# Kernel optimization log

Hardware: AMD Instinct MI355X
Metric: run time of the kernel (lower is better)

## Reference

```python
import jax, jax.numpy as jnp
import numpy as np

B, T, D, H = 32, 4096, 512, 8
HD = D // H
SCALE = HD ** -0.5


def setup_inputs() -> dict:
    key = jax.random.key(0)
    ks = jax.random.split(key, 5)
    s = 0.02
    return {
        "enc": jax.random.normal(ks[0], (B, T, D), dtype=jnp.float32),
        "Wq": jax.random.normal(ks[1], (D, D), dtype=jnp.float32) * s,
        "Wk": jax.random.normal(ks[2], (D, D), dtype=jnp.float32) * s,
        "Wv": jax.random.normal(ks[3], (D, D), dtype=jnp.float32) * s,
        "Wo": jax.random.normal(ks[4], (D, D), dtype=jnp.float32) * s,
    }


def reference(enc, Wq, Wk, Wv, Wo):
    b, t, d = enc.shape
    # projections (torch Linear: y = x @ W.T)
    q = enc[:, -1, :] @ Wq.T                     # [B, D]
    k = (enc @ Wk.T).reshape(b, t, H, HD)        # [B, T, H, HD]
    v = (enc @ Wv.T).reshape(b, t, H, HD)        # [B, T, H, HD]
    q = q.reshape(b, H, HD)                      # [B, H, HD]
    scores = jnp.einsum('bhd,bthd->bht', q, k) * SCALE   # [B, H, T]
    weights = jax.nn.softmax(scores, axis=-1)             # [B, H, T]
    context = jnp.einsum('bht,bthd->bhd', weights, v)     # [B, H, HD]
    context = context.reshape(b, d) @ Wo.T                # [B, D]
    return (context, weights.mean(axis=1))
```

## Files before the change

### kernel.cpp

```cpp
#include <hip/hip_runtime.h>

#define BB 32
#define TT 4096
#define DD 512
#define HH 8
#define HDD 64
#define SCALE_F 0.125f
#define NCHS 64
#define CHUNKS 32
#define TC 128

__global__ __launch_bounds__(256) void k_qu(const float* __restrict__ enc,
                                            const float* __restrict__ Wq,
                                            const float* __restrict__ Wk,
                                            float* __restrict__ u) {
    __shared__ float x[DD];
    __shared__ float qh[HDD];
    int b = blockIdx.x >> 3, h = blockIdx.x & 7;
    int tid = threadIdx.x;
    const float* el = enc + ((size_t)b * TT + (TT - 1)) * DD;
    for (int i = tid; i < DD; i += 256) x[i] = el[i];
    __syncthreads();
    if (tid < HDD) {
        const float4* wr = (const float4*)(Wq + (size_t)(h * HDD + tid) * DD);
        float acc = 0.f;
#pragma unroll 4
        for (int d = 0; d < DD / 4; ++d) {
            float4 w = wr[d];
            acc += w.x * x[4 * d] + w.y * x[4 * d + 1] + w.z * x[4 * d + 2] + w.w * x[4 * d + 3];
        }
        qh[tid] = acc;
    }
    __syncthreads();
#pragma unroll
    for (int k = 0; k < 2; ++k) {
        int d = tid + 256 * k;
        float acc = 0.f;
#pragma unroll 8
        for (int j = 0; j < HDD; ++j)
            acc += qh[j] * Wk[(size_t)(h * HDD + j) * DD + d];
        u[(size_t)(b * HH + h) * DD + d] = acc * SCALE_F;
    }
}

__global__ __launch_bounds__(256) void k_sexp(const float* __restrict__ enc,
                                              const float* __restrict__ u,
                                              float* __restrict__ wt,
                                              float* __restrict__ lsum) {
    __shared__ float stile[HH][66];
    int b = blockIdx.x >> 6;
    int c = blockIdx.x & 63;
    int t0 = c * 64;
    int wave = threadIdx.x >> 6, lane = threadIdx.x & 63;
    int tid = threadIdx.x;
    const float* ub = u + (size_t)b * HH * DD;
    float4 uA[HH], uB[HH];
#pragma unroll
    for (int h = 0; h < HH; ++h) {
        uA[h] = *(const float4*)(ub + h * DD + 4 * lane);
        uB[h] = *(const float4*)(ub + h * DD + 256 + 4 * lane);
    }
    bool b3 = (lane & 8) != 0, b4 = (lane & 16) != 0, b5 = (lane & 32) != 0;
    int myh = ((lane >> 3) & 1) * 4 + ((lane >> 4) & 1) * 2 + ((lane >> 5) & 1);
    for (int tt = wave; tt < 64; tt += 4) {
        int t = t0 + tt;
        const float* row = enc + ((size_t)b * TT + t) * DD;
        float4 e0 = *(const float4*)(row + 4 * lane);
        float4 e1 = *(const float4*)(row + 256 + 4 * lane);
        float a[HH];
#pragma unroll
        for (int h = 0; h < HH; ++h)
            a[h] = uA[h].x * e0.x + uA[h].y * e0.y + uA[h].z * e0.z + uA[h].w * e0.w
                 + uB[h].x * e1.x + uB[h].y * e1.y + uB[h].z * e1.z + uB[h].w * e1.w;
        float s[4];
#pragma unroll
        for (int j = 0; j < 4; ++j) {
            float snd = b3 ? a[j] : a[j + 4];
            float kp  = b3 ? a[j + 4] : a[j];
            s[j] = kp + __shfl_xor(snd, 8, 64);
        }
        float p[2];
#pragma unroll
        for (int j = 0; j < 2; ++j) {
            float snd = b4 ? s[j] : s[j + 2];
            float kp  = b4 ? s[j + 2] : s[j];
            p[j] = kp + __shfl_xor(snd, 16, 64);
        }
        float snd = b5 ? p[0] : p[1];
        float q0 = (b5 ? p[1] : p[0]) + __shfl_xor(snd, 32, 64);
        q0 += __shfl_xor(q0, 1, 64);
        q0 += __shfl_xor(q0, 2, 64);
        q0 += __shfl_xor(q0, 4, 64);
        if ((lane & 7) == 0) stile[myh][tt] = __expf(q0);
    }
    __syncthreads();
#pragma unroll
    for (int k = 0; k < 2; ++k) {
        int idx = tid + 256 * k;
        int h = idx >> 6, tt = idx & 63;
        wt[(size_t)(b * HH + h) * TT + t0 + tt] = stile[h][tt];
    }
    if (tid < HH) {
        float s = 0.f;
#pragma unroll
        for (int t = 0; t < 64; ++t) s += stile[tid][t];
        lsum[(size_t)(b * NCHS + c) * HH + tid] = s;
    }
}

__global__ __launch_bounds__(256) void k_wsum(const float* __restrict__ enc,
                                              const float* __restrict__ wt,
                                              float* __restrict__ partial) {
    __shared__ float wl[HH * TC];
    __shared__ float mrg[HH * DD];
    int b = blockIdx.x / CHUNKS, c = blockIdx.x % CHUNKS;
    int t0 = c * TC, tid = threadIdx.x;
    {
        int h = tid >> 5, i0 = (tid & 31) * 4;
        *(float4*)(wl + h * TC + i0) =
            *(const float4*)(wt + (size_t)(b * HH + h) * TT + t0 + i0);
    }
    __syncthreads();
    int grp = tid >> 7, gl = tid & 127;
    float4 acc[HH];
#pragma unroll
    for (int h = 0; h < HH; ++h) acc[h] = make_float4(0.f, 0.f, 0.f, 0.f);
#pragma unroll 4
    for (int i = 0; i < TC / 2; ++i) {
        int r = grp + 2 * i;
        float4 e = *(const float4*)(enc + ((size_t)b * TT + t0 + r) * DD + gl * 4);
        float w0 = wl[0 * TC + r], w1 = wl[1 * TC + r], w2 = wl[2 * TC + r], w3 = wl[3 * TC + r];
        float w4 = wl[4 * TC + r], w5 = wl[5 * TC + r], w6 = wl[6 * TC + r], w7 = wl[7 * TC + r];
        acc[0].x += w0 * e.x; acc[0].y += w0 * e.y; acc[0].z += w0 * e.z; acc[0].w += w0 * e.w;
        acc[1].x += w1 * e.x; acc[1].y += w1 * e.y; acc[1].z += w1 * e.z; acc[1].w += w1 * e.w;
        acc[2].x += w2 * e.x; acc[2].y += w2 * e.y; acc[2].z += w2 * e.z; acc[2].w += w2 * e.w;
        acc[3].x += w3 * e.x; acc[3].y += w3 * e.y; acc[3].z += w3 * e.z; acc[3].w += w3 * e.w;
        acc[4].x += w4 * e.x; acc[4].y += w4 * e.y; acc[4].z += w4 * e.z; acc[4].w += w4 * e.w;
        acc[5].x += w5 * e.x; acc[5].y += w5 * e.y; acc[5].z += w5 * e.z; acc[5].w += w5 * e.w;
        acc[6].x += w6 * e.x; acc[6].y += w6 * e.y; acc[6].z += w6 * e.z; acc[6].w += w6 * e.w;
        acc[7].x += w7 * e.x; acc[7].y += w7 * e.y; acc[7].z += w7 * e.z; acc[7].w += w7 * e.w;
    }
    if (grp == 1) {
#pragma unroll
        for (int h = 0; h < HH; ++h) *(float4*)(mrg + h * DD + gl * 4) = acc[h];
    }
    __syncthreads();
    if (grp == 0) {
        float* pp = partial + (size_t)(b * CHUNKS + c) * HH * DD + gl * 4;
#pragma unroll
        for (int h = 0; h < HH; ++h) {
            float4 m = *(const float4*)(mrg + h * DD + gl * 4);
            float4 r = acc[h];
            r.x += m.x; r.y += m.y; r.z += m.z; r.w += m.w;
            *(float4*)(pp + h * DD) = r;
        }
    }
}

__global__ __launch_bounds__(256) void k_pred(const float* __restrict__ partial,
                                              const float* __restrict__ lsum,
                                              float* __restrict__ ctx) {
    int idx = blockIdx.x * 256 + threadIdx.x;
    int b = idx >> 10, r4 = (idx & 1023) * 4;
    int h = r4 >> 9;
    float L = 0.f;
#pragma unroll 8
    for (int c = 0; c < NCHS; ++c) L += lsum[(size_t)(b * NCHS + c) * HH + h];
    const float* pp = partial + (size_t)b * CHUNKS * HH * DD + r4;
    float4 acc = make_float4(0.f, 0.f, 0.f, 0.f);
#pragma unroll 8
    for (int c = 0; c < CHUNKS; ++c) {
        float4 v = *(const float4*)(pp + (size_t)c * HH * DD);
        acc.x += v.x; acc.y += v.y; acc.z += v.z; acc.w += v.w;
    }
    float inv = 1.0f / L;
    acc.x *= inv; acc.y *= inv; acc.z *= inv; acc.w *= inv;
    *(float4*)(ctx + (size_t)b * HH * DD + r4) = acc;
}

__global__ __launch_bounds__(256) void k_out1(const float* __restrict__ wt,
                                              const float* __restrict__ lsum,
                                              float* __restrict__ out1) {
    __shared__ float Linv[HH];
    int b = blockIdx.x, tid = threadIdx.x;
    if (tid < HH) {
        float s = 0.f;
#pragma unroll 8
        for (int c = 0; c < NCHS; ++c) s += lsum[(size_t)(b * NCHS + c) * HH + tid];
        Linv[tid] = 0.125f / s;
    }
    __syncthreads();
#pragma unroll
    for (int k = 0; k < TT / 256; ++k) {
        int t = tid + 256 * k;
        float s = 0.f;
#pragma unroll
        for (int h = 0; h < HH; ++h)
            s += wt[(size_t)(b * HH + h) * TT + t] * Linv[h];
        out1[(size_t)b * TT + t] = s;
    }
}

__global__ __launch_bounds__(256) void k_v(const float* __restrict__ ctx,
                                           const float* __restrict__ Wv,
                                           float* __restrict__ ctxv) {
    __shared__ float cs[DD];
    int b = blockIdx.x >> 3, h = blockIdx.x & 7;
    int tid = threadIdx.x;
    for (int i = tid; i < DD; i += 256) cs[i] = ctx[(size_t)b * HH * DD + h * DD + i];
    __syncthreads();
    int out = tid >> 2, q = tid & 3;
    int i = h * HDD + out;
    const float4* wr = (const float4*)(Wv + (size_t)i * DD + q * 128);
    const float* cc = cs + q * 128;
    float acc = 0.f;
#pragma unroll 8
    for (int d = 0; d < 32; ++d) {
        float4 w = wr[d];
        acc += w.x * cc[4 * d] + w.y * cc[4 * d + 1] + w.z * cc[4 * d + 2] + w.w * cc[4 * d + 3];
    }
    acc += __shfl_xor(acc, 1, 64);
    acc += __shfl_xor(acc, 2, 64);
    if (q == 0) ctxv[(size_t)b * DD + i] = acc;
}

__global__ __launch_bounds__(256) void k_o(const float* __restrict__ ctxv,
                                           const float* __restrict__ Wo,
                                           float* __restrict__ out0) {
    __shared__ float cs[DD];
    int b = blockIdx.x >> 3, g = blockIdx.x & 7;
    int tid = threadIdx.x;
    for (int i = tid; i < DD; i += 256) cs[i] = ctxv[(size_t)b * DD + i];
    __syncthreads();
    int out = tid >> 2, q = tid & 3;
    int o = g * HDD + out;
    const float4* wr = (const float4*)(Wo + (size_t)o * DD + q * 128);
    const float* cc = cs + q * 128;
    float acc = 0.f;
#pragma unroll 8
    for (int d = 0; d < 32; ++d) {
        float4 w = wr[d];
        acc += w.x * cc[4 * d] + w.y * cc[4 * d + 1] + w.z * cc[4 * d + 2] + w.w * cc[4 * d + 3];
    }
    acc += __shfl_xor(acc, 1, 64);
    acc += __shfl_xor(acc, 2, 64);
    if (q == 0) out0[(size_t)b * DD + o] = acc;
}

extern "C" void kernel_launch(void* const* d_in, const int* in_sizes, int n_in,
                              void* d_out, int out_size, void* d_ws, size_t ws_size,
                              hipStream_t stream) {
    const float* enc = (const float*)d_in[0];
    const float* Wq  = (const float*)d_in[1];
    const float* Wk  = (const float*)d_in[2];
    const float* Wv  = (const float*)d_in[3];
    const float* Wo  = (const float*)d_in[4];

    float* ws = (float*)d_ws;
    float* u       = ws;
    float* wt      = u + (size_t)BB * HH * DD;
    float* lsum    = wt + (size_t)BB * HH * TT;
    float* partial = lsum + (size_t)BB * NCHS * HH;
    float* ctx     = partial + (size_t)BB * CHUNKS * HH * DD;
    float* ctxv    = ctx + (size_t)BB * HH * DD;

    float* out0 = (float*)d_out;
    float* out1 = out0 + BB * DD;

    hipLaunchKernelGGL(k_qu,    dim3(BB * HH),     dim3(256), 0, stream, enc, Wq, Wk, u);
    hipLaunchKernelGGL(k_sexp,  dim3(BB * NCHS),   dim3(256), 0, stream, enc, u, wt, lsum);
    hipLaunchKernelGGL(k_wsum,  dim3(BB * CHUNKS), dim3(256), 0, stream, enc, wt, partial);
    hipLaunchKernelGGL(k_pred,  dim3(BB * HH * DD / 1024), dim3(256), 0, stream, partial, lsum, ctx);
    hipLaunchKernelGGL(k_v,     dim3(BB * HH),     dim3(256), 0, stream, ctx, Wv, ctxv);
    hipLaunchKernelGGL(k_o,     dim3(BB * HH),     dim3(256), 0, stream, ctxv, Wo, out0);
    hipLaunchKernelGGL(k_out1,  dim3(BB),          dim3(256), 0, stream, wt, lsum, out1);
}
```

Before: 495.3 us.

## Fuse score/exp and weighted-sum passes to read encoder once via LDS tiles

Merges the score+exp kernel and the weighted-value-sum kernel into one kernel. It stages 32-row tiles of enc in shared memory and computes both the exp scores and the per-head weighted sums from the same tile, so the 256MB encoder tensor is read from HBM once instead of twice. The partial reduction and normalisation are folded into the Wv projection kernel. The out1 kernel is split across more blocks for parallelism. The costs are 64KB of LDS per block, which limits occupancy, and extra barriers per tile with no overlap between loads and compute. The softmax also still has no max subtraction.

```diff
diff --git a/kernel.cpp b/kernel.cpp
--- a/kernel.cpp
+++ b/kernel.cpp
@@ -6,9 +6,10 @@
 #define HH 8
 #define HDD 64
 #define SCALE_F 0.125f
-#define NCHS 64
 #define CHUNKS 32
 #define TC 128
+#define TILE 32
+#define NT (TC / TILE)
 
 __global__ __launch_bounds__(256) void k_qu(const float* __restrict__ enc,
                                             const float* __restrict__ Wq,
@@ -43,16 +44,17 @@
     }
 }
 
-__global__ __launch_bounds__(256) void k_sexp(const float* __restrict__ enc,
+__global__ __launch_bounds__(256) void k_main(const float* __restrict__ enc,
                                               const float* __restrict__ u,
                                               float* __restrict__ wt,
-                                              float* __restrict__ lsum) {
-    __shared__ float stile[HH][66];
-    int b = blockIdx.x >> 6;
-    int c = blockIdx.x & 63;
-    int t0 = c * 64;
-    int wave = threadIdx.x >> 6, lane = threadIdx.x & 63;
-    int tid = threadIdx.x;
+                                              float* __restrict__ lsum,
+                                              float* __restrict__ partial) {
+    __shared__ float et[TILE * DD];
+    __shared__ float stile[TILE][HH];
+    int b = blockIdx.x / CHUNKS, c = blockIdx.x % CHUNKS;
+    int t0 = c * TC;
+    int tid = threadIdx.x, wave = tid >> 6, lane = tid & 63;
+
     const float* ub = u + (size_t)b * HH * DD;
     float4 uA[HH], uB[HH];
 #pragma unroll
@@ -62,152 +64,107 @@
     }
     bool b3 = (lane & 8) != 0, b4 = (lane & 16) != 0, b5 = (lane & 32) != 0;
     int myh = ((lane >> 3) & 1) * 4 + ((lane >> 4) & 1) * 2 + ((lane >> 5) & 1);
-    for (int tt = wave; tt < 64; tt += 4) {
-        int t = t0 + tt;
-        const float* row = enc + ((size_t)b * TT + t) * DD;
-        float4 e0 = *(const float4*)(row + 4 * lane);
-        float4 e1 = *(const float4*)(row + 256 + 4 * lane);
-        float a[HH];
-#pragma unroll
-        for (int h = 0; h < HH; ++h)
-            a[h] = uA[h].x * e0.x + uA[h].y * e0.y + uA[h].z * e0.z + uA[h].w * e0.w
-                 + uB[h].x * e1.x + uB[h].y * e1.y + uB[h].z * e1.z + uB[h].w * e1.w;
-        float s[4];
-#pragma unroll
-        for (int j = 0; j < 4; ++j) {
-            float snd = b3 ? a[j] : a[j + 4];
-            float kp  = b3 ? a[j + 4] : a[j];
-            s[j] = kp + __shfl_xor(snd, 8, 64);
-        }
-        float p[2];
-#pragma unroll
-        for (int j = 0; j < 2; ++j) {
-            float snd = b4 ? s[j] : s[j + 2];
-            float kp  = b4 ? s[j + 2] : s[j];
-            p[j] = kp + __shfl_xor(snd, 16, 64);
-        }
-        float snd = b5 ? p[0] : p[1];
-        float q0 = (b5 ? p[1] : p[0]) + __shfl_xor(snd, 32, 64);
-        q0 += __shfl_xor(q0, 1, 64);
-        q0 += __shfl_xor(q0, 2, 64);
-        q0 += __shfl_xor(q0, 4, 64);
-        if ((lane & 7) == 0) stile[myh][tt] = __expf(q0);
-    }
-    __syncthreads();
-#pragma unroll
-    for (int k = 0; k < 2; ++k) {
-        int idx = tid + 256 * k;
-        int h = idx >> 6, tt = idx & 63;
-        wt[(size_t)(b * HH + h) * TT + t0 + tt] = stile[h][tt];
-    }
-    if (tid < HH) {
-        float s = 0.f;
-#pragma unroll
-        for (int t = 0; t < 64; ++t) s += stile[tid][t];
-        lsum[(size_t)(b * NCHS + c) * HH + tid] = s;
-    }
-}
-
-__global__ __launch_bounds__(256) void k_wsum(const float* __restrict__ enc,
-                                              const float* __restrict__ wt,
-                                              float* __restrict__ partial) {
-    __shared__ float wl[HH * TC];
-    __shared__ float mrg[HH * DD];
-    int b = blockIdx.x / CHUNKS, c = blockIdx.x % CHUNKS;
-    int t0 = c * TC, tid = threadIdx.x;
-    {
-        int h = tid >> 5, i0 = (tid & 31) * 4;
-        *(float4*)(wl + h * TC + i0) =
-            *(const float4*)(wt + (size_t)(b * HH + h) * TT + t0 + i0);
-    }
-    __syncthreads();
-    int grp = tid >> 7, gl = tid & 127;
-    float4 acc[HH];
-#pragma unroll
-    for (int h = 0; h < HH; ++h) acc[h] = make_float4(0.f, 0.f, 0.f, 0.f);
+
+    float Lacc = 0.f;
+    float2 acc[HH];
+#pragma unroll
+    for (int h = 0; h < HH; ++h) acc[h] = make_float2(0.f, 0.f);
+    int d0 = tid * 2;
+
+    for (int tile = 0; tile < NT; ++tile) {
+        int tb = t0 + tile * TILE;
+        const float4* gp = (const float4*)(enc + (size_t)(b * TT + tb) * DD);
+        float4* lp = (float4*)et;
+#pragma unroll
+        for (int k = 0; k < 16; ++k) {
+            int idx = tid + 256 * k;
+            lp[idx] = gp[idx];
+        }
+        __syncthreads();
+        for (int tt = wave; tt < TILE; tt += 4) {
+            const float* row = et + tt * DD;
+            float4 e0 = *(const float4*)(row + 4 * lane);
+            float4 e1 = *(const float4*)(row + 256 + 4 * lane);
+            float a[HH];
+#pragma unroll
+            for (int h = 0; h < HH; ++h)
+                a[h] = uA[h].x * e0.x + uA[h].y * e0.y + uA[h].z * e0.z + uA[h].w * e0.w
+                     + uB[h].x * e1.x + uB[h].y * e1.y + uB[h].z * e1.z + uB[h].w * e1.w;
+            float s[4];
+#pragma unroll
+            for (int j = 0; j < 4; ++j) {
+                float snd = b3 ? a[j] : a[j + 4];
+                float kp  = b3 ? a[j + 4] : a[j];
+                s[j] = kp + __shfl_xor(snd, 8, 64);
+            }
+            float p[2];
+#pragma unroll
+            for (int j = 0; j < 2; ++j) {
+                float snd = b4 ? s[j] : s[j + 2];
+                float kp  = b4 ? s[j + 2] : s[j];
+                p[j] = kp + __shfl_xor(snd, 16, 64);
+            }
+            float snd = b5 ? p[0] : p[1];
+            float q0 = (b5 ? p[1] : p[0]) + __shfl_xor(snd, 32, 64);
+            q0 += __shfl_xor(q0, 1, 64);
+            q0 += __shfl_xor(q0, 2, 64);
+            q0 += __shfl_xor(q0, 4, 64);
+            if ((lane & 7) == 0) stile[tt][myh] = __expf(q0);
+        }
+        __syncthreads();
+        {
+            int h = tid >> 5, ttv = tid & 31;
+            wt[(size_t)(b * HH + h) * TT + tb + ttv] = stile[ttv][h];
+        }
+        if (tid < HH) {
+#pragma unroll
+            for (int t = 0; t < TILE; ++t) Lacc += stile[t][tid];
+        }
 #pragma unroll 4
-    for (int i = 0; i < TC / 2; ++i) {
-        int r = grp + 2 * i;
-        float4 e = *(const float4*)(enc + ((size_t)b * TT + t0 + r) * DD + gl * 4);
-        float w0 = wl[0 * TC + r], w1 = wl[1 * TC + r], w2 = wl[2 * TC + r], w3 = wl[3 * TC + r];
-        float w4 = wl[4 * TC + r], w5 = wl[5 * TC + r], w6 = wl[6 * TC + r], w7 = wl[7 * TC + r];
-        acc[0].x += w0 * e.x; acc[0].y += w0 * e.y; acc[0].z += w0 * e.z; acc[0].w += w0 * e.w;
-        acc[1].x += w1 * e.x; acc[1].y += w1 * e.y; acc[1].z += w1 * e.z; acc[1].w += w1 * e.w;
-        acc[2].x += w2 * e.x; acc[2].y += w2 * e.y; acc[2].z += w2 * e.z; acc[2].w += w2 * e.w;
-        acc[3].x += w3 * e.x; acc[3].y += w3 * e.y; acc[3].z += w3 * e.z; acc[3].w += w3 * e.w;
-        acc[4].x += w4 * e.x; acc[4].y += w4 * e.y; acc[4].z += w4 * e.z; acc[4].w += w4 * e.w;
-        acc[5].x += w5 * e.x; acc[5].y += w5 * e.y; acc[5].z += w5 * e.z; acc[5].w += w5 * e.w;
-        acc[6].x += w6 * e.x; acc[6].y += w6 * e.y; acc[6].z += w6 * e.z; acc[6].w += w6 * e.w;
-        acc[7].x += w7 * e.x; acc[7].y += w7 * e.y; acc[7].z += w7 * e.z; acc[7].w += w7 * e.w;
-    }
-    if (grp == 1) {
-#pragma unroll
-        for (int h = 0; h < HH; ++h) *(float4*)(mrg + h * DD + gl * 4) = acc[h];
-    }
-    __syncthreads();
-    if (grp == 0) {
-        float* pp = partial + (size_t)(b * CHUNKS + c) * HH * DD + gl * 4;
-#pragma unroll
-        for (int h = 0; h < HH; ++h) {
-            float4 m = *(const float4*)(mrg + h * DD + gl * 4);
-            float4 r = acc[h];
-            r.x += m.x; r.y += m.y; r.z += m.z; r.w += m.w;
-            *(float4*)(pp + h * DD) = r;
-        }
-    }
-}
-
-__global__ __launch_bounds__(256) void k_pred(const float* __restrict__ partial,
+        for (int r = 0; r < TILE; ++r) {
+            float2 e = *(const float2*)(et + r * DD + d0);
+            const float4* sp = (const float4*)stile[r];
+            float4 w0 = sp[0], w1 = sp[1];
+            acc[0].x += w0.x * e.x; acc[0].y += w0.x * e.y;
+            acc[1].x += w0.y * e.x; acc[1].y += w0.y * e.y;
+            acc[2].x += w0.z * e.x; acc[2].y += w0.z * e.y;
+            acc[3].x += w0.w * e.x; acc[3].y += w0.w * e.y;
+            acc[4].x += w1.x * e.x; acc[4].y += w1.x * e.y;
+            acc[5].x += w1.y * e.x; acc[5].y += w1.y * e.y;
+            acc[6].x += w1.z * e.x; acc[6].y += w1.z * e.y;
+            acc[7].x += w1.w * e.x; acc[7].y += w1.w * e.y;
+        }
+        __syncthreads();
+    }
+    float* pp = partial + (size_t)(b * CHUNKS + c) * HH * DD + d0;
+#pragma unroll
+    for (int h = 0; h < HH; ++h) *(float2*)(pp + h * DD) = acc[h];
+    if (tid < HH) lsum[(size_t)(b * CHUNKS + c) * HH + tid] = Lacc;
+}
+
+__global__ __launch_bounds__(256) void k_vctx(const float* __restrict__ partial,
                                               const float* __restrict__ lsum,
-                                              float* __restrict__ ctx) {
-    int idx = blockIdx.x * 256 + threadIdx.x;
-    int b = idx >> 10, r4 = (idx & 1023) * 4;
-    int h = r4 >> 9;
-    float L = 0.f;
-#pragma unroll 8
-    for (int c = 0; c < NCHS; ++c) L += lsum[(size_t)(b * NCHS + c) * HH + h];
-    const float* pp = partial + (size_t)b * CHUNKS * HH * DD + r4;
-    float4 acc = make_float4(0.f, 0.f, 0.f, 0.f);
+                                              const float* __restrict__ Wv,
+                                              float* __restrict__ ctxv) {
+    __shared__ float cs[DD];
+    __shared__ float Linv;
+    int b = blockIdx.x >> 3, h = blockIdx.x & 7;
+    int tid = threadIdx.x;
+    if (tid == 0) {
+        float L = 0.f;
+#pragma unroll 8
+        for (int c = 0; c < CHUNKS; ++c) L += lsum[(size_t)(b * CHUNKS + c) * HH + h];
+        Linv = 1.0f / L;
+    }
+    float a0 = 0.f, a1 = 0.f;
+    const float* pb = partial + (size_t)(b * CHUNKS) * HH * DD + (size_t)h * DD;
 #pragma unroll 8
     for (int c = 0; c < CHUNKS; ++c) {
-        float4 v = *(const float4*)(pp + (size_t)c * HH * DD);
-        acc.x += v.x; acc.y += v.y; acc.z += v.z; acc.w += v.w;
-    }
-    float inv = 1.0f / L;
-    acc.x *= inv; acc.y *= inv; acc.z *= inv; acc.w *= inv;
-    *(float4*)(ctx + (size_t)b * HH * DD + r4) = acc;
-}
-
-__global__ __launch_bounds__(256) void k_out1(const float* __restrict__ wt,
-                                              const float* __restrict__ lsum,
-                                              float* __restrict__ out1) {
-    __shared__ float Linv[HH];
-    int b = blockIdx.x, tid = threadIdx.x;
-    if (tid < HH) {
-        float s = 0.f;
-#pragma unroll 8
-        for (int c = 0; c < NCHS; ++c) s += lsum[(size_t)(b * NCHS + c) * HH + tid];
-        Linv[tid] = 0.125f / s;
-    }
-    __syncthreads();
-#pragma unroll
-    for (int k = 0; k < TT / 256; ++k) {
-        int t = tid + 256 * k;
-        float s = 0.f;
-#pragma unroll
-        for (int h = 0; h < HH; ++h)
-            s += wt[(size_t)(b * HH + h) * TT + t] * Linv[h];
-        out1[(size_t)b * TT + t] = s;
-    }
-}
-
-__global__ __launch_bounds__(256) void k_v(const float* __restrict__ ctx,
-                                           const float* __restrict__ Wv,
-                                           float* __restrict__ ctxv) {
-    __shared__ float cs[DD];
-    int b = blockIdx.x >> 3, h = blockIdx.x & 7;
-    int tid = threadIdx.x;
-    for (int i = tid; i < DD; i += 256) cs[i] = ctx[(size_t)b * HH * DD + h * DD + i];
+        const float* pp = pb + (size_t)c * HH * DD;
+        a0 += pp[tid]; a1 += pp[tid + 256];
+    }
+    __syncthreads();
+    cs[tid] = a0 * Linv; cs[tid + 256] = a1 * Linv;
     __syncthreads();
     int out = tid >> 2, q = tid & 3;
     int i = h * HDD + out;
@@ -245,6 +202,30 @@
     acc += __shfl_xor(acc, 1, 64);
     acc += __shfl_xor(acc, 2, 64);
     if (q == 0) out0[(size_t)b * DD + o] = acc;
+}
+
+__global__ __launch_bounds__(256) void k_out1(const float* __restrict__ wt,
+                                              const float* __restrict__ lsum,
+                                              float* __restrict__ out1) {
+    __shared__ float Linv[HH];
+    int b = blockIdx.x >> 3, seg = blockIdx.x & 7;
+    int tid = threadIdx.x;
+    if (tid < HH) {
+        float s = 0.f;
+#pragma unroll 8
+        for (int c = 0; c < CHUNKS; ++c) s += lsum[(size_t)(b * CHUNKS + c) * HH + tid];
+        Linv[tid] = 0.125f / s;
+    }
+    __syncthreads();
+#pragma unroll
+    for (int k = 0; k < 2; ++k) {
+        int t = seg * 512 + tid + 256 * k;
+        float s = 0.f;
+#pragma unroll
+        for (int h = 0; h < HH; ++h)
+            s += wt[(size_t)(b * HH + h) * TT + t] * Linv[h];
+        out1[(size_t)b * TT + t] = s;
+    }
 }
 
 extern "C" void kernel_launch(void* const* d_in, const int* in_sizes, int n_in,
@@ -260,18 +241,15 @@
     float* u       = ws;
     float* wt      = u + (size_t)BB * HH * DD;
     float* lsum    = wt + (size_t)BB * HH * TT;
-    float* partial = lsum + (size_t)BB * NCHS * HH;
-    float* ctx     = partial + (size_t)BB * CHUNKS * HH * DD;
-    float* ctxv    = ctx + (size_t)BB * HH * DD;
+    float* partial = lsum + (size_t)BB * CHUNKS * HH;
+    float* ctxv    = partial + (size_t)BB * CHUNKS * HH * DD;
 
     float* out0 = (float*)d_out;
     float* out1 = out0 + BB * DD;
 
     hipLaunchKernelGGL(k_qu,    dim3(BB * HH),     dim3(256), 0, stream, enc, Wq, Wk, u);
-    hipLaunchKernelGGL(k_sexp,  dim3(BB * NCHS),   dim3(256), 0, stream, enc, u, wt, lsum);
-    hipLaunchKernelGGL(k_wsum,  dim3(BB * CHUNKS), dim3(256), 0, stream, enc, wt, partial);
-    hipLaunchKernelGGL(k_pred,  dim3(BB * HH * DD / 1024), dim3(256), 0, stream, partial, lsum, ctx);
-    hipLaunchKernelGGL(k_v,     dim3(BB * HH),     dim3(256), 0, stream, ctx, Wv, ctxv);
+    hipLaunchKernelGGL(k_main,  dim3(BB * CHUNKS), dim3(256), 0, stream, enc, u, wt, lsum, partial);
+    hipLaunchKernelGGL(k_vctx,  dim3(BB * HH),     dim3(256), 0, stream, partial, lsum, Wv, ctxv);
     hipLaunchKernelGGL(k_o,     dim3(BB * HH),     dim3(256), 0, stream, ctxv, Wo, out0);
-    hipLaunchKernelGGL(k_out1,  dim3(BB),          dim3(256), 0, stream, wt, lsum, out1);
-}
+    hipLaunchKernelGGL(k_out1,  dim3(BB * HH),     dim3(256), 0, stream, wt, lsum, out1);
+}
```

Result: faster. 416.5 us (-15.9%).
